# Kernel optimization log

Hardware: AMD Instinct MI355X
Metric: run time of the kernel (lower is better)

The kernel has to match this reference:

```python
import jax, jax.numpy as jnp
import numpy as np
from jax import lax


def _spectral_topk_filter(X, k):
    # X: complex (B, Freq, F). Keep top-k magnitude freqs per (batch, feature).
    Xt = jnp.transpose(X, (0, 2, 1))  # (B, F, Freq)
    mag = jnp.abs(Xt)
    _, idx = lax.top_k(mag, k)  # (B, F, k)
    vals = jnp.take_along_axis(Xt, idx, axis=-1)
    B, F, _ = Xt.shape
    bi = jnp.arange(B)[:, None, None]
    fi = jnp.arange(F)[None, :, None]
    filt = jnp.zeros_like(Xt).at[bi, fi, idx].set(vals)
    return jnp.transpose(filt, (0, 2, 1))  # (B, Freq, F)


def _hamming_periodic(W):
    # matches torch.hamming_window(W) default (periodic=True)
    n = jnp.arange(W, dtype=jnp.float32)
    return 0.54 - 0.46 * jnp.cos(2.0 * jnp.pi * n / W)


def setup_inputs() -> dict:
    key = jax.random.key(0)
    x = jax.random.normal(key, (32, 4096, 128), dtype=jnp.float32)
    return {"x": x, "window_size": 25, "k": 16}


def reference(x, window_size, k):
    B, T, F = x.shape
    W = window_size
    half = W // 2

    # spectral filter: rfft -> keep top-k freqs -> irfft
    X = jnp.fft.rfft(x, axis=1)
    Xf = _spectral_topk_filter(X, k)
    xf = jnp.fft.irfft(Xf, axis=1).astype(x.dtype)  # (B, T, F)

    # flip-padding as in the torch module
    left = xf[:, :half, :][:, ::-1, :]
    right = xf[:, -half:, :][:, ::-1, :]
    xp = jnp.concatenate([left, xf, right], axis=1)  # (B, T + 2*half, F)

    # sliding hamming-window average == depthwise 1D correlation (no kernel flip,
    # matching the elementwise multiply in the original loop)
    w = _hamming_periodic(W).astype(x.dtype)
    xr = jnp.transpose(xp, (0, 2, 1)).reshape(B * F, 1, -1)  # (B*F, 1, Tp)
    out = lax.conv_general_dilated(xr, w[None, None, :], (1,), 'VALID')  # (B*F, 1, T)
    out = out.reshape(B, F, T).transpose(0, 2, 1) / jnp.sum(w)
    return out
```

## Files before the change

kernel.cpp:

```cpp
#include <hip/hip_runtime.h>
#include <math.h>


#define NN     4096
#define LOGN   12
#define NT     256
#define EPT    16
#define KTOP   16
#define WSZ    25
#define HALFW  12
#define FDIM   128
#define BATCH  32
#define RECL   88
#define TT     128
#define TWO_PI 6.283185307179586f

__device__ __forceinline__ int swz(int a) { return a + (a >> 5); }

#define CMUL(r, i, wr_, wi_) { float _r = (r); (r) = _r * (wr_) - (i) * (wi_); (i) = _r * (wi_) + (i) * (wr_); }
#define MULNI(r, i)          { float _r = (r); (r) = (i); (i) = -_r; }

__device__ __forceinline__ void cs_phase(int ph, float& c, float& s)
{
    const float rev = (float)ph * (1.0f / (float)NN);
    s = __builtin_amdgcn_sinf(rev);
    c = __builtin_amdgcn_cosf(rev);
}

__device__ __forceinline__ void dft16(float (&zr)[16], float (&zi)[16])
{
    const float C1 = 0.92387953251128674f;
    const float S1 = 0.38268343236508978f;
    const float R2 = 0.70710678118654752f;
    float yr[16], yi[16];
    #pragma unroll
    for (int n2 = 0; n2 < 4; ++n2) {
        float ar = zr[n2],      ai = zi[n2];
        float br = zr[4 + n2],  bi = zi[4 + n2];
        float cr = zr[8 + n2],  ci = zi[8 + n2];
        float dr = zr[12 + n2], di = zi[12 + n2];
        float t0r = ar + cr, t0i = ai + ci;
        float t1r = ar - cr, t1i = ai - ci;
        float t2r = br + dr, t2i = bi + di;
        float t3r = br - dr, t3i = bi - di;
        yr[n2]      = t0r + t2r;  yi[n2]      = t0i + t2i;
        yr[4 + n2]  = t1r + t3i;  yi[4 + n2]  = t1i - t3r;
        yr[8 + n2]  = t0r - t2r;  yi[8 + n2]  = t0i - t2i;
        yr[12 + n2] = t1r - t3i;  yi[12 + n2] = t1i + t3r;
    }
    CMUL(yr[5],  yi[5],  C1, -S1);
    CMUL(yr[6],  yi[6],  R2, -R2);
    CMUL(yr[7],  yi[7],  S1, -C1);
    CMUL(yr[9],  yi[9],  R2, -R2);
    MULNI(yr[10], yi[10]);
    CMUL(yr[11], yi[11], -R2, -R2);
    CMUL(yr[13], yi[13], S1, -C1);
    CMUL(yr[14], yi[14], -R2, -R2);
    CMUL(yr[15], yi[15], -C1, S1);
    #pragma unroll
    for (int k1 = 0; k1 < 4; ++k1) {
        float ar = yr[k1 * 4 + 0], ai = yi[k1 * 4 + 0];
        float br = yr[k1 * 4 + 1], bi = yi[k1 * 4 + 1];
        float cr = yr[k1 * 4 + 2], ci = yi[k1 * 4 + 2];
        float dr = yr[k1 * 4 + 3], di = yi[k1 * 4 + 3];
        float t0r = ar + cr, t0i = ai + ci;
        float t1r = ar - cr, t1i = ai - ci;
        float t2r = br + dr, t2i = bi + di;
        float t3r = br - dr, t3i = bi - di;
        zr[k1]      = t0r + t2r;  zi[k1]      = t0i + t2i;
        zr[4 + k1]  = t1r + t3i;  zi[4 + k1]  = t1i - t3r;
        zr[8 + k1]  = t0r - t2r;  zi[8 + k1]  = t0i - t2i;
        zr[12 + k1] = t1r - t3i;  zi[12 + k1] = t1i + t3r;
    }
}

__global__ __launch_bounds__(NT, 6)
void spectral_fft_kernel(const float* __restrict__ x, float* __restrict__ ws)
{
    __shared__ float s_x[NN + (NN >> 5)];
    __shared__ float s_w[WSZ];
    __shared__ float s_wsum;
    __shared__ float s_cv[64];
    __shared__ int   s_ck[64];
    __shared__ float s_cr[64];
    __shared__ float s_ci[64];
    __shared__ int   s_kf[KTOP];
    __shared__ float s_kr[KTOP];
    __shared__ float s_ki[KTOP];
    __shared__ float s_vr[KTOP];
    __shared__ float s_vi[KTOP];
    __shared__ float s_cd2[KTOP];
    __shared__ float s_edge[2 * HALFW];
    __shared__ float s_dl[2 * HALFW];

    const int tid = threadIdx.x;

    const int p  = blockIdx.x;
    const int wg = ((p & 7) << 9) + (p >> 3);
    const int b  = wg >> 7;
    const int f  = wg & (FDIM - 1);
    const float* xc = x + (size_t)b * NN * FDIM + f;

    if (tid < WSZ)
        s_w[tid] = 0.54f - 0.46f * cosf(TWO_PI * (float)tid / (float)WSZ);

    float zr[16], zi[16];
    #pragma unroll
    for (int r = 0; r < 16; ++r) { zr[r] = xc[(tid + (r << 8)) * FDIM]; zi[r] = 0.0f; }

    dft16(zr, zi);

    if (tid == 0) {
        float a = 0.0f;
        for (int i = 0; i < WSZ; ++i) a += s_w[i];
        s_wsum = a;
    }

    const int b0 = ((tid >> 4) << 8) + (tid & 15);

    {
        float sn, cs;
        sincosf(-TWO_PI * (float)tid / (float)NN, &sn, &cs);
        float dr = cs, di = sn;
        float wr = dr, wi = di;
        #pragma unroll
        for (int u = 1; u < 16; ++u) {
            CMUL(zr[u], zi[u], wr, wi);
            float nr = wr * dr - wi * di; wi = wr * di + wi * dr; wr = nr;
        }
    }
    #pragma unroll
    for (int u = 0; u < 16; ++u) s_x[swz(tid + (u << 8))] = zr[u];
    __syncthreads();
    #pragma unroll
    for (int r = 0; r < 16; ++r) zr[r] = s_x[swz(b0 + (r << 4))];
    __syncthreads();
    #pragma unroll
    for (int u = 0; u < 16; ++u) s_x[swz(tid + (u << 8))] = zi[u];
    __syncthreads();
    #pragma unroll
    for (int r = 0; r < 16; ++r) zi[r] = s_x[swz(b0 + (r << 4))];

    dft16(zr, zi);
    {
        const int pp = tid & 15;
        float sn, cs;
        sincosf(-TWO_PI * (float)(pp << 4) / (float)NN, &sn, &cs);
        float dr = cs, di = sn;
        float wr = dr, wi = di;
        #pragma unroll
        for (int u = 1; u < 16; ++u) {
            CMUL(zr[u], zi[u], wr, wi);
            float nr = wr * dr - wi * di; wi = wr * di + wi * dr; wr = nr;
        }
    }
    __syncthreads();
    #pragma unroll
    for (int u = 0; u < 16; ++u) s_x[swz(b0 + (u << 4))] = zr[u];
    __syncthreads();
    #pragma unroll
    for (int r = 0; r < 16; ++r) zr[r] = s_x[swz((tid << 4) + r)];
    __syncthreads();
    #pragma unroll
    for (int u = 0; u < 16; ++u) s_x[swz(b0 + (u << 4))] = zi[u];
    __syncthreads();
    #pragma unroll
    for (int r = 0; r < 16; ++r) zi[r] = s_x[swz((tid << 4) + r)];

    dft16(zr, zi);

    const int fbase = ((tid & 15) << 4) | (tid >> 4);
    float mg[9];
    float lmax = -1.0f; int lk = 0x7fffffff;
    #pragma unroll
    for (int u = 0; u < 9; ++u) {
        float v = zr[u] * zr[u] + zi[u] * zi[u];
        if (u == 8 && fbase != 0) v = -1.0f;
        mg[u] = v;
        if (v > lmax) { lmax = v; lk = (u << 8) + fbase; }
    }

    const int lane = tid & 63;
    const int wid  = tid >> 6;
    for (int r = 0; r < KTOP; ++r) {
        float bv = lmax; int bk = lk;
        #pragma unroll
        for (int off = 1; off < 64; off <<= 1) {
            float ov = __shfl_xor(bv, off);
            int   ok = __shfl_xor(bk, off);
            if (ov > bv || (ov == bv && ok < bk)) { bv = ov; bk = ok; }
        }
        if (lmax == bv && lk == bk) {
            const int uw = bk >> 8;
            #pragma unroll
            for (int u2 = 0; u2 < 9; ++u2) {
                if (u2 == uw) { s_cr[wid * 16 + r] = zr[u2]; s_ci[wid * 16 + r] = zi[u2]; mg[u2] = -1.0f; }
            }
            lmax = -1.0f; lk = 0x7fffffff;
            #pragma unroll
            for (int u2 = 0; u2 < 9; ++u2) {
                float v = mg[u2];
                if (v > lmax) { lmax = v; lk = (u2 << 8) + fbase; }
            }
        }
        if (lane == r) { s_cv[wid * 16 + r] = bv; s_ck[wid * 16 + r] = bk; }
    }
    __syncthreads();

    if (tid < 64) {
        float cv = s_cv[tid]; int ck = s_ck[tid];
        float cr = s_cr[tid], ci = s_ci[tid];
        for (int r = 0; r < KTOP; ++r) {
            float bv = cv; int bk = ck;
            #pragma unroll
            for (int off = 1; off < 64; off <<= 1) {
                float ov = __shfl_xor(bv, off);
                int   ok = __shfl_xor(bk, off);
                if (ov > bv || (ov == bv && ok < bk)) { bv = ov; bk = ok; }
            }
            if (cv == bv && ck == bk) {
                s_kf[r] = bk; s_kr[r] = cr; s_ki[r] = ci;
                cv = -1.0f; ck = 0x7fffffff;
            }
        }
    }
    __syncthreads();

    if (tid < 2 * HALFW) {
        const int te = (tid < HALFW) ? tid : (NN - 2 * HALFW + tid);
        float a = 0.0f;
        for (int r = 0; r < KTOP; ++r) {
            const int fj = s_kf[r];
            float vr = s_kr[r], vi = s_ki[r];
            if (fj == 0 || fj == NN / 2) { vi = 0.0f; }
            else { vr *= 2.0f; vi *= 2.0f; }
            float c, s;
            cs_phase((fj * te) & (NN - 1), c, s);
            a += vr * c - vi * s;
        }
        s_edge[tid] = a * (1.0f / (float)NN);
    }
    if (tid >= 64 && tid < 64 + KTOP) {
        const int r = tid - 64;
        const int fj = s_kf[r];
        float vr = s_kr[r], vi = s_ki[r];
        float sc;
        if (fj == 0 || fj == NN / 2) { vi = 0.0f; sc = 1.0f; }
        else                         { sc = 2.0f; }
        float cr, ci, dc, ds;
        cs_phase((-HALFW * fj) & (NN - 1), cr, ci);
        cs_phase(fj, dc, ds);
        float hr = 0.0f, hi = 0.0f;
        for (int i = 0; i < WSZ; ++i) {
            const float wv = s_w[i];
            hr += wv * cr; hi += wv * ci;
            float nc = cr * dc - ci * ds;
            ci = ci * dc + cr * ds;
            cr = nc;
        }
        const float scale = sc / ((float)NN * s_wsum);
        s_vr[r]  = (vr * hr - vi * hi) * scale;
        s_vi[r]  = (vr * hi + vi * hr) * scale;
        s_cd2[r] = dc + dc;
    }
    __syncthreads();

    if (tid == 0) {
        const float rinv = 1.0f / s_wsum;
        for (int t = 0; t < HALFW; ++t) {
            float d = 0.0f;
            for (int i = 0; t + i < HALFW; ++i)
                d += s_w[i] * (s_edge[HALFW - 1 - t - i] - s_edge[HALFW + t + i]);
            s_dl[t] = d * rinv;
        }
        for (int j = 0; j < HALFW; ++j) {
            float d = 0.0f;
            for (int i = 2 * HALFW - j; i < WSZ; ++i)
                d += s_w[i] * (s_edge[4 * HALFW - 1 - j - i] - s_edge[j + i - 2 * HALFW]);
            s_dl[HALFW + j] = d * rinv;
        }
    }
    __syncthreads();

    if (tid < RECL) {
        float v;
        if      (tid < 16) v = s_vr[tid];
        else if (tid < 32) v = s_vi[tid - 16];
        else if (tid < 48) v = s_cd2[tid - 32];
        else if (tid < 64) v = (float)s_kf[tid - 48];
        else               v = s_dl[tid - 64];
        ws[(size_t)wg * RECL + tid] = v;
    }
}

__global__ __launch_bounds__(NT, 4)
void spectral_recon_kernel(const float* __restrict__ ws, float* __restrict__ out)
{
    __shared__ float s_c[FDIM * 65];

    const int tid = threadIdx.x;
    const int tb  = blockIdx.x * TT;
    const int b   = blockIdx.y;
    const int chB = b * FDIM;

    #pragma unroll
    for (int k = 0; k < (FDIM * 64) / NT; ++k) {
        int idx = tid + (k << 8);
        int ch  = idx >> 6;
        int j   = idx & 63;
        s_c[ch * 65 + j] = ws[(size_t)(chB + ch) * RECL + j];
    }
    __syncthreads();

    const int m  = tid & 31;
    const int tq = tid >> 5;
    const int t0 = tb + tq * 16;

    #pragma unroll 1
    for (int c = 0; c < 4; ++c) {
        const int ch = c * 32 + m;
        const float* rec = &s_c[ch * 65];

        float acc[16];
        #pragma unroll
        for (int i = 0; i < 16; ++i) acc[i] = 0.0f;

        for (int r = 0; r < KTOP; ++r) {
            const float vr  = rec[r];
            const float vi  = rec[16 + r];
            const float cd2 = rec[32 + r];
            const int   fj  = (int)rec[48 + r];
            const int   p0  = (fj * t0) & (NN - 1);
            float c0, s0, cm, sm;
            cs_phase(p0, c0, s0);
            cs_phase((p0 - fj) & (NN - 1), cm, sm);
            float g1 = vr * c0 - vi * s0;
            float g0 = vr * cm - vi * sm;
            #pragma unroll
            for (int i = 0; i < 16; ++i) {
                acc[i] += g1;
                const float gn = __builtin_fmaf(cd2, g1, -g0);
                g0 = g1; g1 = gn;
            }
        }

        if (tb == 0 && tq == 0) {
            #pragma unroll
            for (int i = 0; i < HALFW; ++i)
                acc[i] += ws[(size_t)(chB + ch) * RECL + 64 + i];
        }
        if (tb == NN - TT && tq == 7) {
            #pragma unroll
            for (int i = 4; i < 16; ++i)
                acc[i] += ws[(size_t)(chB + ch) * RECL + 76 + (i - 4)];
        }
        const size_t obase = ((size_t)b * NN + t0) * FDIM + ch;
        #pragma unroll
        for (int i = 0; i < 16; ++i)
            out[obase + (size_t)i * FDIM] = acc[i];
    }
}

__global__ __launch_bounds__(NT, 3)
void spectral_filter_fallback(const float* __restrict__ x, float* __restrict__ out)
{
    __shared__ float s_re[NN + (NN >> 5)];
    __shared__ float s_im[NN];
    __shared__ float s_tw[NN];
    __shared__ float s_w[WSZ];
    __shared__ float s_wsum;
    __shared__ float s_rv[NT / 64];
    __shared__ int   s_ri[NT / 64];
    __shared__ int   s_kf[KTOP];
    __shared__ float s_kr[KTOP];
    __shared__ float s_ki[KTOP];

    const int tid = threadIdx.x;
    const int c   = blockIdx.x;
    const int b   = c >> 7;
    const int f   = c & (FDIM - 1);
    const size_t base = (size_t)b * NN * FDIM + f;

    if (tid < WSZ)
        s_w[tid] = 0.54f - 0.46f * cosf(TWO_PI * (float)tid / (float)WSZ);

    for (int i = tid; i < NN / 2; i += NT) {
        float sn, cs;
        sincosf(-TWO_PI * (float)i / (float)NN, &sn, &cs);
        s_tw[i]          = cs;
        s_tw[i + NN / 2] = sn;
    }

    #pragma unroll
    for (int i = 0; i < EPT; ++i) {
        int j = tid + i * NT;
        int t = (int)(__brev((unsigned)j) >> (32 - LOGN));
        s_re[j] = x[base + (size_t)t * FDIM];
        s_im[j] = 0.0f;
    }
    __syncthreads();

    if (tid == 0) {
        float a = 0.0f;
        for (int i = 0; i < WSZ; ++i) a += s_w[i];
        s_wsum = a;
    }

    for (int s = 1; s <= LOGN; ++s) {
        const int half = 1 << (s - 1);
        const int tsh  = LOGN - s;
        #pragma unroll
        for (int i = 0; i < EPT / 2; ++i) {
            int j  = tid + i * NT;
            int p  = j & (half - 1);
            int i0 = ((j >> (s - 1)) << s) + p;
            int i1 = i0 + half;
            int q  = p << tsh;
            float wr = s_tw[q], wi = s_tw[q + NN / 2];
            float ar = s_re[i0], ai = s_im[i0];
            float br = s_re[i1], bi = s_im[i1];
            float tr = br * wr - bi * wi;
            float ti = br * wi + bi * wr;
            s_re[i0] = ar + tr;  s_im[i0] = ai + ti;
            s_re[i1] = ar - tr;  s_im[i1] = ai - ti;
        }
        __syncthreads();
    }

    for (int i = tid; i < NN / 2 + 1; i += NT) {
        float rr = s_re[i], ii = s_im[i];
        s_tw[i] = rr * rr + ii * ii;
    }
    __syncthreads();

    for (int r = 0; r < KTOP; ++r) {
        float best = -1.0f; int bidx = 0x7fffffff;
        for (int i = tid; i < NN / 2 + 1; i += NT) {
            float v = s_tw[i];
            if (v > best) { best = v; bidx = i; }
        }
        #pragma unroll
        for (int off = 32; off > 0; off >>= 1) {
            float ov = __shfl_down(best, off);
            int   oi = __shfl_down(bidx, off);
            if (ov > best || (ov == best && oi < bidx)) { best = ov; bidx = oi; }
        }
        const int wid = tid >> 6;
        if ((tid & 63) == 0) { s_rv[wid] = best; s_ri[wid] = bidx; }
        __syncthreads();
        if (tid == 0) {
            float bv = s_rv[0]; int bx = s_ri[0];
            #pragma unroll
            for (int w2 = 1; w2 < NT / 64; ++w2) {
                float ov = s_rv[w2]; int oi = s_ri[w2];
                if (ov > bv || (ov == bv && oi < bx)) { bv = ov; bx = oi; }
            }
            s_kf[r] = bx;
            s_kr[r] = s_re[bx];
            s_ki[r] = s_im[bx];
            s_tw[bx] = -1.0f;
        }
        __syncthreads();
    }

    const int t0 = tid * EPT;
    float xf[EPT];
    #pragma unroll
    for (int i = 0; i < EPT; ++i) xf[i] = 0.0f;

    for (int r = 0; r < KTOP; ++r) {
        const int fj = s_kf[r];
        float vr = s_kr[r], vi = s_ki[r];
        float sc = 2.0f;
        if (fj == 0 || fj == NN / 2) { sc = 1.0f; vi = 0.0f; }
        vr *= sc; vi *= sc;
        const int ph0 = (fj * t0) & (NN - 1);
        float c0, s0, dc, ds;
        sincosf((float)ph0 * (TWO_PI / (float)NN), &s0, &c0);
        sincosf((float)fj  * (TWO_PI / (float)NN), &ds, &dc);
        float cr = c0, ci = s0;
        #pragma unroll
        for (int i = 0; i < EPT; ++i) {
            xf[i] += vr * cr - vi * ci;
            float nc = cr * dc - ci * ds;
            ci = ci * dc + cr * ds;
            cr = nc;
        }
    }
    __syncthreads();

    #pragma unroll
    for (int i = 0; i < EPT; ++i)
        s_re[swz(t0 + i)] = xf[i] * (1.0f / (float)NN);
    __syncthreads();

    float win[EPT + WSZ - 1];
    #pragma unroll
    for (int i = 0; i < EPT + WSZ - 1; ++i) {
        int a = t0 + i - HALFW;
        if (a < 0)        a = -1 - a;
        else if (a >= NN) a = 2 * NN - 1 - a;
        win[i] = s_re[swz(a)];
    }

    const float rinv = 1.0f / s_wsum;
    float acc[EPT];
    #pragma unroll
    for (int t = 0; t < EPT; ++t) acc[t] = 0.0f;
    #pragma unroll
    for (int i = 0; i < WSZ; ++i) {
        const float wv = s_w[i];
        #pragma unroll
        for (int t = 0; t < EPT; ++t) acc[t] += win[t + i] * wv;
    }
    #pragma unroll
    for (int t = 0; t < EPT; ++t)
        out[base + (size_t)(t0 + t) * FDIM] = acc[t] * rinv;
}

extern "C" void kernel_launch(void* const* d_in, const int* in_sizes, int n_in,
                              void* d_out, int out_size, void* d_ws, size_t ws_size,
                              hipStream_t stream)
{
    const float* x = (const float*)d_in[0];
    float* out = (float*)d_out;
    const size_t need = (size_t)BATCH * FDIM * RECL * sizeof(float);
    if (ws_size >= need) {
        float* ws = (float*)d_ws;
        spectral_fft_kernel<<<dim3(BATCH * FDIM), NT, 0, stream>>>(x, ws);
        spectral_recon_kernel<<<dim3(NN / TT, BATCH), NT, 0, stream>>>(ws, out);
    } else {
        spectral_filter_fallback<<<dim3(BATCH * FDIM), NT, 0, stream>>>(x, out);
    }
}
```

Before: 227.4 us.

## Interleave four channels in recon recurrence and precompute per-frequency step twiddles

```diff
diff --git a/kernel.cpp b/kernel.cpp
--- a/kernel.cpp
+++ b/kernel.cpp
@@ -11,7 +11,8 @@
 #define HALFW  12
 #define FDIM   128
 #define BATCH  32
-#define RECL   88
+#define RECL   120
+#define HOTF   96
 #define TT     128
 #define TWO_PI 6.283185307179586f
 
@@ -74,7 +75,7 @@
     }
 }
 
-__global__ __launch_bounds__(NT, 6)
+__global__ __launch_bounds__(NT, 8)
 void spectral_fft_kernel(const float* __restrict__ x, float* __restrict__ ws)
 {
     __shared__ float s_x[NN + (NN >> 5)];
@@ -90,6 +91,8 @@
     __shared__ float s_vr[KTOP];
     __shared__ float s_vi[KTOP];
     __shared__ float s_cd2[KTOP];
+    __shared__ float s_dc[KTOP];
+    __shared__ float s_ds[KTOP];
     __shared__ float s_edge[2 * HALFW];
     __shared__ float s_dl[2 * HALFW];
 
@@ -262,6 +265,8 @@
         s_vr[r]  = (vr * hr - vi * hi) * scale;
         s_vi[r]  = (vr * hi + vi * hr) * scale;
         s_cd2[r] = dc + dc;
+        s_dc[r]  = dc;
+        s_ds[r]  = ds;
     }
     __syncthreads();
 
@@ -284,19 +289,21 @@
 
     if (tid < RECL) {
         float v;
-        if      (tid < 16) v = s_vr[tid];
-        else if (tid < 32) v = s_vi[tid - 16];
-        else if (tid < 48) v = s_cd2[tid - 32];
-        else if (tid < 64) v = (float)s_kf[tid - 48];
-        else               v = s_dl[tid - 64];
+        if      (tid < 16)  v = s_vr[tid];
+        else if (tid < 32)  v = s_vi[tid - 16];
+        else if (tid < 48)  v = s_cd2[tid - 32];
+        else if (tid < 64)  v = (float)s_kf[tid - 48];
+        else if (tid < 88)  v = s_dl[tid - 64];
+        else if (tid < 104) v = s_dc[tid - 88];
+        else                v = s_ds[tid - 104];
         ws[(size_t)wg * RECL + tid] = v;
     }
 }
 
-__global__ __launch_bounds__(NT, 4)
+__global__ __launch_bounds__(NT, 3)
 void spectral_recon_kernel(const float* __restrict__ ws, float* __restrict__ out)
 {
-    __shared__ float s_c[FDIM * 65];
+    __shared__ float s_c[FDIM * (HOTF + 1)];
 
     const int tid = threadIdx.x;
     const int tb  = blockIdx.x * TT;
@@ -304,11 +311,12 @@
     const int chB = b * FDIM;
 
     #pragma unroll
-    for (int k = 0; k < (FDIM * 64) / NT; ++k) {
-        int idx = tid + (k << 8);
-        int ch  = idx >> 6;
-        int j   = idx & 63;
-        s_c[ch * 65 + j] = ws[(size_t)(chB + ch) * RECL + j];
+    for (int k = 0; k < (FDIM * HOTF) / NT; ++k) {
+        int idx = tid + k * NT;
+        int ch  = idx / HOTF;
+        int j   = idx - ch * HOTF;
+        int gj  = (j < 64) ? j : (j + 24);
+        s_c[ch * (HOTF + 1) + j] = ws[(size_t)(chB + ch) * RECL + gj];
     }
     __syncthreads();
 
@@ -316,48 +324,59 @@
     const int tq = tid >> 5;
     const int t0 = tb + tq * 16;
 
-    #pragma unroll 1
+    float acc[4][16];
+    #pragma unroll
+    for (int c = 0; c < 4; ++c)
+        #pragma unroll
+        for (int i = 0; i < 16; ++i) acc[c][i] = 0.0f;
+
+    for (int r = 0; r < KTOP; ++r) {
+        float g1v[4], g0v[4], cdv[4];
+        #pragma unroll
+        for (int c = 0; c < 4; ++c) {
+            const float* rec = &s_c[(c * 32 + m) * (HOTF + 1)];
+            const float vr  = rec[r];
+            const float vi  = rec[16 + r];
+            cdv[c]          = rec[32 + r];
+            const int   fj  = (int)rec[48 + r];
+            const float dc  = rec[64 + r];
+            const float ds  = rec[80 + r];
+            const int   p0  = (fj * t0) & (NN - 1);
+            float c0, s0;
+            cs_phase(p0, c0, s0);
+            const float cm = c0 * dc + s0 * ds;
+            const float sm = s0 * dc - c0 * ds;
+            g1v[c] = vr * c0 - vi * s0;
+            g0v[c] = vr * cm - vi * sm;
+        }
+        #pragma unroll
+        for (int i = 0; i < 16; ++i) {
+            #pragma unroll
+            for (int c = 0; c < 4; ++c) {
+                acc[c][i] += g1v[c];
+                const float gn = __builtin_fmaf(cdv[c], g1v[c], -g0v[c]);
+                g0v[c] = g1v[c]; g1v[c] = gn;
+            }
+        }
+    }
+
+    #pragma unroll
     for (int c = 0; c < 4; ++c) {
         const int ch = c * 32 + m;
-        const float* rec = &s_c[ch * 65];
-
-        float acc[16];
-        #pragma unroll
-        for (int i = 0; i < 16; ++i) acc[i] = 0.0f;
-
-        for (int r = 0; r < KTOP; ++r) {
-            const float vr  = rec[r];
-            const float vi  = rec[16 + r];
-            const float cd2 = rec[32 + r];
-            const int   fj  = (int)rec[48 + r];
-            const int   p0  = (fj * t0) & (NN - 1);
-            float c0, s0, cm, sm;
-            cs_phase(p0, c0, s0);
-            cs_phase((p0 - fj) & (NN - 1), cm, sm);
-            float g1 = vr * c0 - vi * s0;
-            float g0 = vr * cm - vi * sm;
-            #pragma unroll
-            for (int i = 0; i < 16; ++i) {
-                acc[i] += g1;
-                const float gn = __builtin_fmaf(cd2, g1, -g0);
-                g0 = g1; g1 = gn;
-            }
-        }
-
         if (tb == 0 && tq == 0) {
             #pragma unroll
             for (int i = 0; i < HALFW; ++i)
-                acc[i] += ws[(size_t)(chB + ch) * RECL + 64 + i];
+                acc[c][i] += ws[(size_t)(chB + ch) * RECL + 64 + i];
         }
         if (tb == NN - TT && tq == 7) {
             #pragma unroll
             for (int i = 4; i < 16; ++i)
-                acc[i] += ws[(size_t)(chB + ch) * RECL + 76 + (i - 4)];
+                acc[c][i] += ws[(size_t)(chB + ch) * RECL + 76 + (i - 4)];
         }
         const size_t obase = ((size_t)b * NN + t0) * FDIM + ch;
         #pragma unroll
         for (int i = 0; i < 16; ++i)
-            out[obase + (size_t)i * FDIM] = acc[i];
+            out[obase + (size_t)i * FDIM] = acc[c][i];
     }
 }
 
```

After: 243.4 us. 7.0% more time.

## Retile reconstruction kernel by channel groups and replace second sincos with rotation

Applied to the files above, without the earlier changes.

```diff
diff --git a/kernel.cpp b/kernel.cpp
--- a/kernel.cpp
+++ b/kernel.cpp
@@ -11,8 +11,9 @@
 #define HALFW  12
 #define FDIM   128
 #define BATCH  32
-#define RECL   88
-#define TT     128
+#define RECL   120
+#define CHG    16
+#define TTG    256
 #define TWO_PI 6.283185307179586f
 
 __device__ __forceinline__ int swz(int a) { return a + (a >> 5); }
@@ -74,7 +75,7 @@
     }
 }
 
-__global__ __launch_bounds__(NT, 6)
+__global__ __launch_bounds__(NT, 8)
 void spectral_fft_kernel(const float* __restrict__ x, float* __restrict__ ws)
 {
     __shared__ float s_x[NN + (NN >> 5)];
@@ -90,6 +91,8 @@
     __shared__ float s_vr[KTOP];
     __shared__ float s_vi[KTOP];
     __shared__ float s_cd2[KTOP];
+    __shared__ float s_dc[KTOP];
+    __shared__ float s_ds[KTOP];
     __shared__ float s_edge[2 * HALFW];
     __shared__ float s_dl[2 * HALFW];
 
@@ -262,6 +265,8 @@
         s_vr[r]  = (vr * hr - vi * hi) * scale;
         s_vi[r]  = (vr * hi + vi * hr) * scale;
         s_cd2[r] = dc + dc;
+        s_dc[r]  = dc;
+        s_ds[r]  = ds;
     }
     __syncthreads();
 
@@ -284,81 +289,81 @@
 
     if (tid < RECL) {
         float v;
-        if      (tid < 16) v = s_vr[tid];
-        else if (tid < 32) v = s_vi[tid - 16];
-        else if (tid < 48) v = s_cd2[tid - 32];
-        else if (tid < 64) v = (float)s_kf[tid - 48];
-        else               v = s_dl[tid - 64];
+        if      (tid < 16)  v = s_vr[tid];
+        else if (tid < 32)  v = s_vi[tid - 16];
+        else if (tid < 48)  v = s_cd2[tid - 32];
+        else if (tid < 64)  v = (float)s_kf[tid - 48];
+        else if (tid < 88)  v = s_dl[tid - 64];
+        else if (tid < 104) v = s_dc[tid - 88];
+        else                v = s_ds[tid - 104];
         ws[(size_t)wg * RECL + tid] = v;
     }
 }
 
-__global__ __launch_bounds__(NT, 4)
+__global__ __launch_bounds__(NT, 6)
 void spectral_recon_kernel(const float* __restrict__ ws, float* __restrict__ out)
 {
-    __shared__ float s_c[FDIM * 65];
+    __shared__ float s_rec[CHG][RECL + 1];
 
     const int tid = threadIdx.x;
-    const int tb  = blockIdx.x * TT;
+    const int bx  = blockIdx.x;
+    const int fg  = bx >> 4;
+    const int tt  = bx & 15;
     const int b   = blockIdx.y;
-    const int chB = b * FDIM;
-
-    #pragma unroll
-    for (int k = 0; k < (FDIM * 64) / NT; ++k) {
-        int idx = tid + (k << 8);
-        int ch  = idx >> 6;
-        int j   = idx & 63;
-        s_c[ch * 65 + j] = ws[(size_t)(chB + ch) * RECL + j];
-    }
-    __syncthreads();
-
-    const int m  = tid & 31;
-    const int tq = tid >> 5;
-    const int t0 = tb + tq * 16;
-
-    #pragma unroll 1
-    for (int c = 0; c < 4; ++c) {
-        const int ch = c * 32 + m;
-        const float* rec = &s_c[ch * 65];
-
-        float acc[16];
-        #pragma unroll
-        for (int i = 0; i < 16; ++i) acc[i] = 0.0f;
-
-        for (int r = 0; r < KTOP; ++r) {
-            const float vr  = rec[r];
-            const float vi  = rec[16 + r];
-            const float cd2 = rec[32 + r];
-            const int   fj  = (int)rec[48 + r];
-            const int   p0  = (fj * t0) & (NN - 1);
-            float c0, s0, cm, sm;
-            cs_phase(p0, c0, s0);
-            cs_phase((p0 - fj) & (NN - 1), cm, sm);
-            float g1 = vr * c0 - vi * s0;
-            float g0 = vr * cm - vi * sm;
-            #pragma unroll
-            for (int i = 0; i < 16; ++i) {
-                acc[i] += g1;
-                const float gn = __builtin_fmaf(cd2, g1, -g0);
-                g0 = g1; g1 = gn;
-            }
-        }
-
-        if (tb == 0 && tq == 0) {
-            #pragma unroll
-            for (int i = 0; i < HALFW; ++i)
-                acc[i] += ws[(size_t)(chB + ch) * RECL + 64 + i];
-        }
-        if (tb == NN - TT && tq == 7) {
-            #pragma unroll
-            for (int i = 4; i < 16; ++i)
-                acc[i] += ws[(size_t)(chB + ch) * RECL + 76 + (i - 4)];
-        }
-        const size_t obase = ((size_t)b * NN + t0) * FDIM + ch;
-        #pragma unroll
-        for (int i = 0; i < 16; ++i)
-            out[obase + (size_t)i * FDIM] = acc[i];
-    }
+    const int ch0 = b * FDIM + fg * CHG;
+
+    for (int idx = tid; idx < CHG * RECL; idx += NT) {
+        int ch = idx / RECL;
+        int j  = idx - ch * RECL;
+        s_rec[ch][j] = ws[(size_t)ch0 * RECL + idx];
+    }
+    __syncthreads();
+
+    const int m  = tid & 15;
+    const int tq = tid >> 4;
+    const int t0 = tt * TTG + tq * 16;
+
+    const float* rec = s_rec[m];
+
+    float acc[16];
+    #pragma unroll
+    for (int i = 0; i < 16; ++i) acc[i] = 0.0f;
+
+    for (int r = 0; r < KTOP; ++r) {
+        const float vr  = rec[r];
+        const float vi  = rec[16 + r];
+        const float cd2 = rec[32 + r];
+        const int   fj  = (int)rec[48 + r];
+        const float dc  = rec[88 + r];
+        const float ds  = rec[104 + r];
+        const int   p0  = (fj * t0) & (NN - 1);
+        float c0, s0;
+        cs_phase(p0, c0, s0);
+        const float cm = c0 * dc + s0 * ds;
+        const float sm = s0 * dc - c0 * ds;
+        float g1 = vr * c0 - vi * s0;
+        float g0 = vr * cm - vi * sm;
+        #pragma unroll
+        for (int i = 0; i < 16; ++i) {
+            acc[i] += g1;
+            const float gn = __builtin_fmaf(cd2, g1, -g0);
+            g0 = g1; g1 = gn;
+        }
+    }
+
+    if (tt == 0 && tq == 0) {
+        #pragma unroll
+        for (int i = 0; i < HALFW; ++i) acc[i] += rec[64 + i];
+    }
+    if (tt == 15 && tq == 15) {
+        #pragma unroll
+        for (int i = 4; i < 16; ++i) acc[i] += rec[76 + (i - 4)];
+    }
+
+    const size_t obase = ((size_t)b * NN + t0) * FDIM + fg * CHG + m;
+    #pragma unroll
+    for (int i = 0; i < 16; ++i)
+        out[obase + (size_t)i * FDIM] = acc[i];
 }
 
 __global__ __launch_bounds__(NT, 3)
@@ -528,7 +533,7 @@
     if (ws_size >= need) {
         float* ws = (float*)d_ws;
         spectral_fft_kernel<<<dim3(BATCH * FDIM), NT, 0, stream>>>(x, ws);
-        spectral_recon_kernel<<<dim3(NN / TT, BATCH), NT, 0, stream>>>(ws, out);
+        spectral_recon_kernel<<<dim3((FDIM / CHG) * (NN / TTG), BATCH), NT, 0, stream>>>(ws, out);
     } else {
         spectral_filter_fallback<<<dim3(BATCH * FDIM), NT, 0, stream>>>(x, out);
     }
```

Result: slower. 232.7 us (median of 2 runs) (+2.3%).
